# Kernel tuning notes

Hardware: AMD Instinct MI355X
Metric: run time of the kernel (lower is better)

## Reference

```python
import jax, jax.numpy as jnp
import numpy as np

MIN_SCORE = 0.3       # min_score_threshold
NMS_THRESHOLD = 0.3   # nms_threshold
MAX_OUT = 256         # fixed output padding (jit-compatible replacement for dynamic K)


def _cxcywh_to_xyxy(b):
    cx, cy, w, h = b[..., 0], b[..., 1], b[..., 2], b[..., 3]
    half_w, half_h = w * 0.5, h * 0.5
    return jnp.stack([cx - half_w, cy - half_h, cx + half_w, cy + half_h], axis=-1)


def _pairwise_iou(a, b):
    # a: [N,4], b: [M,4] in xyxy
    lt = jnp.maximum(a[:, None, :2], b[None, :, :2])
    rb = jnp.minimum(a[:, None, 2:], b[None, :, 2:])
    wh = jnp.clip(rb - lt, 0.0)
    inter = wh[..., 0] * wh[..., 1]
    area_a = (a[:, 2] - a[:, 0]) * (a[:, 3] - a[:, 1])
    area_b = (b[:, 2] - b[:, 0]) * (b[:, 3] - b[:, 1])
    return inter / (area_a[:, None] + area_b[None, :] - inter + 1e-9)


def setup_inputs() -> dict:
    key = jax.random.key(0)
    k1, k2 = jax.random.split(key)
    N, n_coords = 8192, 16
    score = jax.random.uniform(k1, (N, 1), dtype=jnp.float32)
    box = jax.random.uniform(k2, (N, n_coords), dtype=jnp.float32)
    return {"score": score, "box": box}


def reference(score, box):
    # score: [N,1], box: [N,n_coords]; single class (n_classes==1, cls=None)
    s = score[:, 0]
    valid = s >= MIN_SCORE                      # score mask applied before NMS
    order = jnp.argsort(-s)                     # score-descending (batched_nms order)
    s_s = s[order]
    v_s = valid[order]
    box_s = box[order]
    bbox = _cxcywh_to_xyxy(box_s[:, :4]).astype(jnp.float32)
    iou = _pairwise_iou(bbox, bbox)             # [N,N]
    N = s.shape[0]

    def body(kept, i):
        # suppressed if overlaps any already-kept (higher-score) box
        suppressed = jnp.any(kept & (iou[:, i] > NMS_THRESHOLD))
        keep_i = v_s[i] & jnp.logical_not(suppressed)
        return kept.at[i].set(keep_i), None

    kept, _ = jax.lax.scan(body, jnp.zeros((N,), dtype=bool), jnp.arange(N))

    # compact kept detections to the front, preserving score order (stable sort)
    comp = jnp.argsort(jnp.where(kept, 0, 1), stable=True)[:MAX_OUT]
    out_valid = kept[comp]                      # [MAX_OUT]
    score_out = jnp.where(out_valid[:, None], s_s[comp][:, None], 0.0)   # [MAX_OUT,1]
    box_out = jnp.where(out_valid[:, None], box_s[comp], 0.0)            # [MAX_OUT,n_coords]
    return score_out, box_out, out_valid
```

## Files before the change

kernel.cpp:

```cpp
#include <hip/hip_runtime.h>
#include <stdint.h>

typedef unsigned long long u64;

#define N 8192
#define NW 128
#define MAX_OUT 256
#define MASK_BYTES ((size_t)N * NW * 8)


__global__ __launch_bounds__(256)
void build_keys_kernel(const float* __restrict__ score, u64* __restrict__ keys,
                       int* __restrict__ rank, int* __restrict__ partial) {
    int i = blockIdx.x * 256 + threadIdx.x;
    float s = score[i];
    uint32_t b = __float_as_uint(s);
    keys[i] = ((u64)(~b) << 32) | (uint32_t)i;
    rank[i] = 0;
    int c = (s >= 0.3f) ? 1 : 0;
    for (int off = 32; off; off >>= 1) c += __shfl_down(c, off);
    __shared__ int part[4];
    if ((threadIdx.x & 63) == 0) part[threadIdx.x >> 6] = c;
    __syncthreads();
    if (threadIdx.x == 0) partial[blockIdx.x] = part[0] + part[1] + part[2] + part[3];
}

__global__ __launch_bounds__(256)
void rank_kernel(const u64* __restrict__ keys, int* __restrict__ rank,
                 const int* __restrict__ partial, int* __restrict__ nvalid) {
    __shared__ u64 kj[1024];
    const int tid = threadIdx.x;
    if (blockIdx.x == 0 && blockIdx.y == 0 && tid < 64) {
        int v = (tid < 32) ? partial[tid] : 0;
        for (int off = 32; off; off >>= 1) v += __shfl_down(v, off);
        if (tid == 0) *nvalid = v;
    }
    const int jbase = blockIdx.y * 1024;
    for (int t = tid; t < 1024; t += 256) kj[t] = keys[jbase + t];
    __syncthreads();
    const int i = blockIdx.x * 256 + tid;
    const u64 ki = keys[i];
    int c = 0;
    #pragma unroll 8
    for (int j = 0; j < 1024; ++j) c += (kj[j] < ki) ? 1 : 0;
    atomicAdd(&rank[i], c);
}

__global__ __launch_bounds__(256)
void scatter_kernel(const float* __restrict__ score, const float* __restrict__ box,
                    const int* __restrict__ rank, int* __restrict__ order,
                    float* __restrict__ s_s, float4* __restrict__ bbox,
                    float* __restrict__ area) {
    int i = blockIdx.x * 256 + threadIdx.x;
    int r = rank[i];
    float s = score[i];
    order[r] = i;
    s_s[r] = s;
    float4 cb = ((const float4*)box)[i * 4];
    float hw = cb.z * 0.5f, hh = cb.w * 0.5f;
    float x0 = cb.x - hw, y0 = cb.y - hh, x1 = cb.x + hw, y1 = cb.y + hh;
    bbox[r] = make_float4(x0, y0, x1, y1);
    area[r] = (x1 - x0) * (y1 - y0);
}

__global__ __launch_bounds__(256)
void mask_kernel(const float4* __restrict__ bbox, const float* __restrict__ area,
                 const int* __restrict__ nvalid_p, u64* __restrict__ mask) {
    const int w = blockIdx.x;
    const int i = blockIdx.y * 256 + threadIdx.x;
    __shared__ float4 jb[64];
    __shared__ float  ja[64];
    if (threadIdx.x < 64) {
        jb[threadIdx.x] = bbox[w * 64 + threadIdx.x];
        ja[threadIdx.x] = area[w * 64 + threadIdx.x];
    }
    __syncthreads();
    const int nv = *nvalid_p;
    if (i >= nv) return;
    if (w < (i >> 6)) return;
    float4 a = bbox[i];
    float  aa = area[i];
    u64 bits = 0;
    #pragma unroll 8
    for (int jj = 0; jj < 64; ++jj) {
        float4 b = jb[jj];
        float lx = fmaxf(a.x, b.x), ly = fmaxf(a.y, b.y);
        float rx = fminf(a.z, b.z), ry = fminf(a.w, b.w);
        float ww = fmaxf(rx - lx, 0.0f), hh = fmaxf(ry - ly, 0.0f);
        float inter = ww * hh;
        float denom = ((aa + ja[jj]) - inter) + 1e-9f;
        float iou = inter / denom;
        bits |= ((u64)(iou > 0.3f)) << jj;
    }
    mask[(size_t)i * NW + w] = bits;
}


struct Pipe { u64 col, s1, s2, g0, g1, g2, g3; };

__device__ __forceinline__ unsigned or_dpp32(unsigned v) {
    v |= (unsigned)__builtin_amdgcn_update_dpp(0, (int)v, 0x111, 0xf, 0xf, true);
    v |= (unsigned)__builtin_amdgcn_update_dpp(0, (int)v, 0x112, 0xf, 0xf, true);
    v |= (unsigned)__builtin_amdgcn_update_dpp(0, (int)v, 0x114, 0xf, 0xf, true);
    v |= (unsigned)__builtin_amdgcn_update_dpp(0, (int)v, 0x118, 0xf, 0xf, true);
    v |= (unsigned)__builtin_amdgcn_update_dpp(0, (int)v, 0x142, 0xf, 0xf, true);
    v |= (unsigned)__builtin_amdgcn_update_dpp(0, (int)v, 0x143, 0xf, 0xf, true);
    return v;
}

__device__ __forceinline__ u64 wave_or64(u64 v) {
    unsigned lo = or_dpp32((unsigned)v);
    unsigned hi = or_dpp32((unsigned)(v >> 32));
    unsigned slo = (unsigned)__builtin_amdgcn_readlane((int)lo, 63);
    unsigned shi = (unsigned)__builtin_amdgcn_readlane((int)hi, 63);
    return ((u64)shi << 32) | (u64)slo;
}

__global__ __launch_bounds__(64)
void nms_kernel(const u64* __restrict__ mask, const float* __restrict__ s_s,
                const int* __restrict__ order, const float* __restrict__ box,
                const int* __restrict__ nvalid_p, float* __restrict__ out) {
    const int lane = threadIdx.x;
    const int nv = *nvalid_p;
    const int nblk = (nv + 63) >> 6;
    __shared__ int kpos[MAX_OUT];
    int kcount = 0;
    u64 s1m = 0, s2m = 0, s2m_old = 0;

    Pipe A, B;
    A.col = A.s1 = A.s2 = A.g0 = A.g1 = A.g2 = A.g3 = 0;
    B.col = B.s1 = B.s2 = B.g0 = B.g1 = B.g2 = B.g3 = 0;
    if (nblk > 0) {
        const u64* r = mask + (size_t)lane * NW;
        A.col = r[0];
        if (nblk > 1) A.s1 = r[1];
        if (nblk > 2) A.s2 = r[2];
    }
    if (nblk > 1) {
        const u64* r = mask + (size_t)(64 + lane) * NW;
        B.col = r[1];
        if (nblk > 2) B.s1 = r[2];
        if (nblk > 3) B.s2 = r[3];
    }

    auto step = [&](int b, Pipe& P) -> bool {
        u64 col = P.col, s1v = P.s1, s2v = P.s2;
        u64 x = P.g0 | P.g1 | P.g2 | P.g3 | s1m | s2m_old;
        const int b2 = b + 2;
        P.col = P.s1 = P.s2 = P.g0 = P.g1 = P.g2 = P.g3 = 0;
        if (b2 < nblk) {
            const u64* r = mask + (size_t)((b2 << 6) + lane) * NW;
            P.col = r[b2];
            if (b2 + 1 < nblk) P.s1 = r[b2 + 1];
            if (b2 + 2 < nblk) P.s2 = r[b2 + 2];
            const int kc = kcount;
            if (lane < kc)       P.g0 = mask[(size_t)kpos[lane]       * NW + b2];
            if (lane +  64 < kc) P.g1 = mask[(size_t)kpos[lane +  64] * NW + b2];
            if (lane + 128 < kc) P.g2 = mask[(size_t)kpos[lane + 128] * NW + b2];
            if (lane + 192 < kc) P.g3 = mask[(size_t)kpos[lane + 192] * NW + b2];
        }
        u64 rw = wave_or64(x);
        const int base = b << 6;
        const int rem = nv - base;
        u64 validm = (rem >= 64) ? ~0ull : ((1ull << rem) - 1ull);
        u64 todo = validm & ~rw;
        u64 km = 0;
        while (todo) {
            int l = (int)__builtin_ctzll(todo);
            u64 row_l = __ballot(((col >> l) & 1ull) != 0);
            if (lane == 0) kpos[kcount] = base + l;
            km |= (1ull << l);
            kcount++;
            todo &= ~row_l;
            todo &= ~(1ull << l);
            if (kcount >= MAX_OUT) break;
        }
        u64 keepm = ((km >> lane) & 1ull) ? ~0ull : 0ull;
        s2m_old = s2m;
        s2m = s2v & keepm;
        s1m = s1v & keepm;
        return kcount < MAX_OUT;
    };

    bool run = true;
    for (int b = 0; run && b < nblk; b += 2) {
        run = step(b, A);
        if (run && b + 1 < nblk) run = step(b + 1, B);
    }

    __syncthreads();
    float* out_score = out;
    float* out_box   = out + MAX_OUT;
    float* out_valid = out + MAX_OUT + MAX_OUT * 16;
    const float4* box4 = (const float4*)box;
    float4* ob4 = (float4*)out_box;
    for (int t = lane; t < MAX_OUT; t += 64) {
        if (t < kcount) {
            int p = kpos[t];
            out_score[t] = s_s[p];
            out_valid[t] = 1.0f;
            int oi = order[p];
            #pragma unroll
            for (int q = 0; q < 4; ++q) ob4[t * 4 + q] = box4[oi * 4 + q];
        } else {
            out_score[t] = 0.0f;
            out_valid[t] = 0.0f;
            float4 z = make_float4(0.f, 0.f, 0.f, 0.f);
            #pragma unroll
            for (int q = 0; q < 4; ++q) ob4[t * 4 + q] = z;
        }
    }
}

extern "C" void kernel_launch(void* const* d_in, const int* in_sizes, int n_in,
                              void* d_out, int out_size, void* d_ws, size_t ws_size,
                              hipStream_t stream) {
    const float* score = (const float*)d_in[0];
    const float* box   = (const float*)d_in[1];
    char* ws = (char*)d_ws;
    u64*    mask    = (u64*)ws;
    u64*    keys    = (u64*)ws;
    int*    rank    = (int*)(ws + 65536);
    int*    partial = (int*)(ws + 98304);
    int*    order  = (int*)   (ws + MASK_BYTES);
    float*  s_s    = (float*) (ws + MASK_BYTES + 32768);
    float4* bbox   = (float4*)(ws + MASK_BYTES + 65536);
    float*  area   = (float*) (ws + MASK_BYTES + 65536 + 131072);
    int*    nvalid = (int*)   (ws + MASK_BYTES + 65536 + 131072 + 32768);

    build_keys_kernel<<<32, 256, 0, stream>>>(score, keys, rank, partial);
    rank_kernel<<<dim3(32, 8), 256, 0, stream>>>(keys, rank, partial, nvalid);
    scatter_kernel<<<32, 256, 0, stream>>>(score, box, rank, order, s_s, bbox, area);
    mask_kernel<<<dim3(128, 32), 256, 0, stream>>>(bbox, area, nvalid, mask);
    nms_kernel<<<1, 64, 0, stream>>>(mask, s_s, order, box, nvalid, (float*)d_out);
}
```

Before: 139.1 us.

## Fuse sort stages into one kernel, transpose mask, avoid IoU division

Replaces the three-kernel key/rank/scatter pipeline with one kernel per 32 elements. Each block loads all scores into shared memory, ranks them by comparison counts and scatters the sorted boxes itself, which removes two launches and the atomics. The IoU mask is stored column-major so the NMS kernel's per-block loads and gathers of kept rows become contiguous. The IoU division is replaced by an fma comparison, with an exact division fallback for near-threshold cases, and whole blocks skip early when they fall outside the triangle or valid range. In exchange, every block redundantly loads all 8192 scores.

```diff
diff --git a/kernel.cpp b/kernel.cpp
--- a/kernel.cpp
+++ b/kernel.cpp
@@ -9,65 +9,76 @@
 #define MASK_BYTES ((size_t)N * NW * 8)
 
 
-__global__ __launch_bounds__(256)
-void build_keys_kernel(const float* __restrict__ score, u64* __restrict__ keys,
-                       int* __restrict__ rank, int* __restrict__ partial) {
-    int i = blockIdx.x * 256 + threadIdx.x;
-    float s = score[i];
-    uint32_t b = __float_as_uint(s);
-    keys[i] = ((u64)(~b) << 32) | (uint32_t)i;
-    rank[i] = 0;
-    int c = (s >= 0.3f) ? 1 : 0;
+__global__ __launch_bounds__(1024)
+void rank_fused_kernel(const float* __restrict__ score, const float* __restrict__ box,
+                       int* __restrict__ order, float* __restrict__ s_s,
+                       float4* __restrict__ bbox, float* __restrict__ area,
+                       int* __restrict__ nvalid) {
+    __shared__ uint32_t ksc[N];
+    __shared__ int psum[32][33];
+    __shared__ int vpart[16];
+    const int tid = threadIdx.x;
+
+    const float4* s4 = (const float4*)score;
+    float4 a = s4[tid * 2], b = s4[tid * 2 + 1];
+    ksc[tid * 8 + 0] = __float_as_uint(a.x);
+    ksc[tid * 8 + 1] = __float_as_uint(a.y);
+    ksc[tid * 8 + 2] = __float_as_uint(a.z);
+    ksc[tid * 8 + 3] = __float_as_uint(a.w);
+    ksc[tid * 8 + 4] = __float_as_uint(b.x);
+    ksc[tid * 8 + 5] = __float_as_uint(b.y);
+    ksc[tid * 8 + 6] = __float_as_uint(b.z);
+    ksc[tid * 8 + 7] = __float_as_uint(b.w);
+    int c = (a.x >= 0.3f) + (a.y >= 0.3f) + (a.z >= 0.3f) + (a.w >= 0.3f)
+          + (b.x >= 0.3f) + (b.y >= 0.3f) + (b.z >= 0.3f) + (b.w >= 0.3f);
     for (int off = 32; off; off >>= 1) c += __shfl_down(c, off);
-    __shared__ int part[4];
-    if ((threadIdx.x & 63) == 0) part[threadIdx.x >> 6] = c;
-    __syncthreads();
-    if (threadIdx.x == 0) partial[blockIdx.x] = part[0] + part[1] + part[2] + part[3];
-}
-
-__global__ __launch_bounds__(256)
-void rank_kernel(const u64* __restrict__ keys, int* __restrict__ rank,
-                 const int* __restrict__ partial, int* __restrict__ nvalid) {
-    __shared__ u64 kj[1024];
-    const int tid = threadIdx.x;
-    if (blockIdx.x == 0 && blockIdx.y == 0 && tid < 64) {
-        int v = (tid < 32) ? partial[tid] : 0;
-        for (int off = 32; off; off >>= 1) v += __shfl_down(v, off);
-        if (tid == 0) *nvalid = v;
-    }
-    const int jbase = blockIdx.y * 1024;
-    for (int t = tid; t < 1024; t += 256) kj[t] = keys[jbase + t];
-    __syncthreads();
-    const int i = blockIdx.x * 256 + tid;
-    const u64 ki = keys[i];
-    int c = 0;
+    if ((tid & 63) == 0) vpart[tid >> 6] = c;
+    __syncthreads();
+    if (blockIdx.x == 0 && tid == 0) {
+        int t = 0;
+        #pragma unroll
+        for (int w = 0; w < 16; ++w) t += vpart[w];
+        *nvalid = t;
+    }
+
+    const int i_local = tid & 31;
+    const int jg = tid >> 5;
+    const int ibase = blockIdx.x * 32;
+    const uint32_t si = ksc[ibase + i_local];
+    const int i = ibase + i_local;
+    int cnt = 0;
+    const int j0 = jg * 256;
     #pragma unroll 8
-    for (int j = 0; j < 1024; ++j) c += (kj[j] < ki) ? 1 : 0;
-    atomicAdd(&rank[i], c);
-}
-
-__global__ __launch_bounds__(256)
-void scatter_kernel(const float* __restrict__ score, const float* __restrict__ box,
-                    const int* __restrict__ rank, int* __restrict__ order,
-                    float* __restrict__ s_s, float4* __restrict__ bbox,
-                    float* __restrict__ area) {
-    int i = blockIdx.x * 256 + threadIdx.x;
-    int r = rank[i];
-    float s = score[i];
-    order[r] = i;
-    s_s[r] = s;
-    float4 cb = ((const float4*)box)[i * 4];
-    float hw = cb.z * 0.5f, hh = cb.w * 0.5f;
-    float x0 = cb.x - hw, y0 = cb.y - hh, x1 = cb.x + hw, y1 = cb.y + hh;
-    bbox[r] = make_float4(x0, y0, x1, y1);
-    area[r] = (x1 - x0) * (y1 - y0);
+    for (int t = 0; t < 256; ++t) {
+        const int j = j0 + t;
+        const uint32_t sj = ksc[j];
+        cnt += (sj > si || (sj == si && j < i)) ? 1 : 0;
+    }
+    psum[i_local][jg] = cnt;
+    __syncthreads();
+
+    if (tid < 32) {
+        int r = 0;
+        #pragma unroll
+        for (int k = 0; k < 32; ++k) r += psum[tid][k];
+        const int ii = ibase + tid;
+        order[r] = ii;
+        s_s[r] = score[ii];
+        float4 cb = ((const float4*)box)[ii * 4];
+        float hw = cb.z * 0.5f, hh = cb.w * 0.5f;
+        float x0 = cb.x - hw, y0 = cb.y - hh, x1 = cb.x + hw, y1 = cb.y + hh;
+        bbox[r] = make_float4(x0, y0, x1, y1);
+        area[r] = (x1 - x0) * (y1 - y0);
+    }
 }
 
 __global__ __launch_bounds__(256)
 void mask_kernel(const float4* __restrict__ bbox, const float* __restrict__ area,
-                 const int* __restrict__ nvalid_p, u64* __restrict__ mask) {
+                 const int* __restrict__ nvalid_p, u64* __restrict__ maskT) {
     const int w = blockIdx.x;
-    const int i = blockIdx.y * 256 + threadIdx.x;
+    if (w < (int)(blockIdx.y << 2)) return;
+    const int nv = *nvalid_p;
+    if ((int)(blockIdx.y * 256) >= nv) return;
     __shared__ float4 jb[64];
     __shared__ float  ja[64];
     if (threadIdx.x < 64) {
@@ -75,26 +86,39 @@
         ja[threadIdx.x] = area[w * 64 + threadIdx.x];
     }
     __syncthreads();
-    const int nv = *nvalid_p;
+    const int i = blockIdx.y * 256 + threadIdx.x;
     if (i >= nv) return;
     if (w < (i >> 6)) return;
-    float4 a = bbox[i];
+    float4 aa4 = bbox[i];
     float  aa = area[i];
-    u64 bits = 0;
+    u64 bits = 0, fb = 0;
     #pragma unroll 8
     for (int jj = 0; jj < 64; ++jj) {
         float4 b = jb[jj];
-        float lx = fmaxf(a.x, b.x), ly = fmaxf(a.y, b.y);
-        float rx = fminf(a.z, b.z), ry = fminf(a.w, b.w);
+        float lx = fmaxf(aa4.x, b.x), ly = fmaxf(aa4.y, b.y);
+        float rx = fminf(aa4.z, b.z), ry = fminf(aa4.w, b.w);
         float ww = fmaxf(rx - lx, 0.0f), hh = fmaxf(ry - ly, 0.0f);
         float inter = ww * hh;
         float denom = ((aa + ja[jj]) - inter) + 1e-9f;
-        float iou = inter / denom;
-        bits |= ((u64)(iou > 0.3f)) << jj;
-    }
-    mask[(size_t)i * NW + w] = bits;
-}
-
+        float d = fmaf(-0.3f, denom, inter);
+        bits |= ((u64)(d > 0.0f)) << jj;
+        fb   |= ((u64)(fabsf(d) <= 1e-5f * denom)) << jj;
+    }
+    if (fb) {
+        while (fb) {
+            int jj = (int)__builtin_ctzll(fb); fb &= fb - 1;
+            float4 b = jb[jj];
+            float lx = fmaxf(aa4.x, b.x), ly = fmaxf(aa4.y, b.y);
+            float rx = fminf(aa4.z, b.z), ry = fminf(aa4.w, b.w);
+            float ww = fmaxf(rx - lx, 0.0f), hh = fmaxf(ry - ly, 0.0f);
+            float inter = ww * hh;
+            float denom = ((aa + ja[jj]) - inter) + 1e-9f;
+            float iou = inter / denom;
+            bits = (bits & ~(1ull << jj)) | (((u64)(iou > 0.3f)) << jj);
+        }
+    }
+    maskT[(size_t)w * N + i] = bits;
+}
 
 struct Pipe { u64 col, s1, s2, g0, g1, g2, g3; };
 
@@ -117,7 +141,7 @@
 }
 
 __global__ __launch_bounds__(64)
-void nms_kernel(const u64* __restrict__ mask, const float* __restrict__ s_s,
+void nms_kernel(const u64* __restrict__ maskT, const float* __restrict__ s_s,
                 const int* __restrict__ order, const float* __restrict__ box,
                 const int* __restrict__ nvalid_p, float* __restrict__ out) {
     const int lane = threadIdx.x;
@@ -131,16 +155,14 @@
     A.col = A.s1 = A.s2 = A.g0 = A.g1 = A.g2 = A.g3 = 0;
     B.col = B.s1 = B.s2 = B.g0 = B.g1 = B.g2 = B.g3 = 0;
     if (nblk > 0) {
-        const u64* r = mask + (size_t)lane * NW;
-        A.col = r[0];
-        if (nblk > 1) A.s1 = r[1];
-        if (nblk > 2) A.s2 = r[2];
+        A.col = maskT[lane];
+        if (nblk > 1) A.s1 = maskT[(size_t)1 * N + lane];
+        if (nblk > 2) A.s2 = maskT[(size_t)2 * N + lane];
     }
     if (nblk > 1) {
-        const u64* r = mask + (size_t)(64 + lane) * NW;
-        B.col = r[1];
-        if (nblk > 2) B.s1 = r[2];
-        if (nblk > 3) B.s2 = r[3];
+        B.col = maskT[(size_t)1 * N + 64 + lane];
+        if (nblk > 2) B.s1 = maskT[(size_t)2 * N + 64 + lane];
+        if (nblk > 3) B.s2 = maskT[(size_t)3 * N + 64 + lane];
     }
 
     auto step = [&](int b, Pipe& P) -> bool {
@@ -149,15 +171,16 @@
         const int b2 = b + 2;
         P.col = P.s1 = P.s2 = P.g0 = P.g1 = P.g2 = P.g3 = 0;
         if (b2 < nblk) {
-            const u64* r = mask + (size_t)((b2 << 6) + lane) * NW;
-            P.col = r[b2];
-            if (b2 + 1 < nblk) P.s1 = r[b2 + 1];
-            if (b2 + 2 < nblk) P.s2 = r[b2 + 2];
+            const int row = (b2 << 6) + lane;
+            P.col = maskT[(size_t)b2 * N + row];
+            if (b2 + 1 < nblk) P.s1 = maskT[(size_t)(b2 + 1) * N + row];
+            if (b2 + 2 < nblk) P.s2 = maskT[(size_t)(b2 + 2) * N + row];
             const int kc = kcount;
-            if (lane < kc)       P.g0 = mask[(size_t)kpos[lane]       * NW + b2];
-            if (lane +  64 < kc) P.g1 = mask[(size_t)kpos[lane +  64] * NW + b2];
-            if (lane + 128 < kc) P.g2 = mask[(size_t)kpos[lane + 128] * NW + b2];
-            if (lane + 192 < kc) P.g3 = mask[(size_t)kpos[lane + 192] * NW + b2];
+            const u64* colw = maskT + (size_t)b2 * N;
+            if (lane < kc)       P.g0 = colw[kpos[lane]];
+            if (lane +  64 < kc) P.g1 = colw[kpos[lane +  64]];
+            if (lane + 128 < kc) P.g2 = colw[kpos[lane + 128]];
+            if (lane + 192 < kc) P.g3 = colw[kpos[lane + 192]];
         }
         u64 rw = wave_or64(x);
         const int base = b << 6;
@@ -218,19 +241,14 @@
     const float* score = (const float*)d_in[0];
     const float* box   = (const float*)d_in[1];
     char* ws = (char*)d_ws;
-    u64*    mask    = (u64*)ws;
-    u64*    keys    = (u64*)ws;
-    int*    rank    = (int*)(ws + 65536);
-    int*    partial = (int*)(ws + 98304);
+    u64*    maskT  = (u64*)ws;
     int*    order  = (int*)   (ws + MASK_BYTES);
     float*  s_s    = (float*) (ws + MASK_BYTES + 32768);
     float4* bbox   = (float4*)(ws + MASK_BYTES + 65536);
     float*  area   = (float*) (ws + MASK_BYTES + 65536 + 131072);
     int*    nvalid = (int*)   (ws + MASK_BYTES + 65536 + 131072 + 32768);
 
-    build_keys_kernel<<<32, 256, 0, stream>>>(score, keys, rank, partial);
-    rank_kernel<<<dim3(32, 8), 256, 0, stream>>>(keys, rank, partial, nvalid);
-    scatter_kernel<<<32, 256, 0, stream>>>(score, box, rank, order, s_s, bbox, area);
-    mask_kernel<<<dim3(128, 32), 256, 0, stream>>>(bbox, area, nvalid, mask);
-    nms_kernel<<<1, 64, 0, stream>>>(mask, s_s, order, box, nvalid, (float*)d_out);
-}
+    rank_fused_kernel<<<256, 1024, 0, stream>>>(score, box, order, s_s, bbox, area, nvalid);
+    mask_kernel<<<dim3(128, 32), 256, 0, stream>>>(bbox, area, nvalid, maskT);
+    nms_kernel<<<1, 64, 0, stream>>>(maskT, s_s, order, box, nvalid, (float*)d_out);
+}
```

Result: faster. 124.2 us (median of 2 runs) (-10.7%).
